# Optimization experiments

Measured on AMD Instinct MI355X. Metric: run time of the kernel, lower is better.

## Reference

```python
import jax, jax.numpy as jnp
import numpy as np

NEG_SLOPE = 0.2  # PyG GATConv default negative_slope


def gat_conv(x, src, dst, W, a_src, a_dst, b, n_nodes):
    # x: [N, Cin]; W: [H, Cin, Cout]; a_src/a_dst: [H, Cout]; b: [Cout]
    xh = jnp.einsum('ni,hio->nho', x, W)                 # [N, H, Cout]
    al_s = jnp.einsum('nho,ho->nh', xh, a_src)           # [N, H]
    al_d = jnp.einsum('nho,ho->nh', xh, a_dst)           # [N, H]
    e = jax.nn.leaky_relu(al_s[src] + al_d[dst], NEG_SLOPE)  # [E, H]
    # softmax over incoming edges of each dst node (self-loops guarantee >=1 edge)
    m = jax.ops.segment_max(e, dst, num_segments=n_nodes)
    ex = jnp.exp(e - m[dst])
    den = jax.ops.segment_sum(ex, dst, num_segments=n_nodes)
    alpha = ex / den[dst]                                # [E, H]
    msg = alpha[:, :, None] * xh[src]                    # [E, H, Cout]
    out = jax.ops.segment_sum(msg, dst, num_segments=n_nodes)  # [N, H, Cout]
    return out.mean(axis=1) + b                          # concat=False -> head mean


def setup_inputs() -> dict:
    key = jax.random.key(0)
    ks = jax.random.split(key, 16)
    N, E, C, H = 20000, 320000, 128, 4
    s = 1.0 / np.sqrt(C)
    inp = {
        'x': jax.random.normal(ks[0], (N, C), dtype=jnp.float32),
        'edge_index': jax.random.randint(ks[1], (2, E), 0, N, dtype=jnp.int64),
    }
    for i, name in enumerate(['1', '2', 'r']):
        k0, k1, k2 = jax.random.split(ks[2 + i], 3)
        inp['W' + name] = jax.random.normal(k0, (H, C, C), dtype=jnp.float32) * s
        inp['as' + name] = jax.random.normal(k1, (H, C), dtype=jnp.float32) * s
        inp['ad' + name] = jax.random.normal(k2, (H, C), dtype=jnp.float32) * s
        inp['b' + name] = jnp.zeros((C,), dtype=jnp.float32)
    return inp


def reference(x, edge_index, W1, as1, ad1, b1, W2, as2, ad2, b2, Wr, asr, adr, br):
    n = x.shape[0]
    loop = jnp.arange(n, dtype=edge_index.dtype)
    src = jnp.concatenate([edge_index[0], loop])  # PyG add_self_loops=True
    dst = jnp.concatenate([edge_index[1], loop])
    h = gat_conv(x, src, dst, W1, as1, ad1, b1, n)
    h = gat_conv(h, src, dst, W2, as2, ad2, b2, n)
    res = gat_conv(x, src, dst, Wr, asr, adr, br, n)
    return h + res
```

## Files before the change

kernel.cpp:

```cpp
#include <hip/hip_runtime.h>
#include <math.h>

#define C 128

typedef unsigned short u16;
typedef __attribute__((ext_vector_type(8))) short short8;
typedef __attribute__((ext_vector_type(4))) float f32x4;
typedef __attribute__((ext_vector_type(4))) u16 u16x4;

__device__ __forceinline__ float b2f(u16 u) {
    union { unsigned i; float f; } x; x.i = (unsigned)u << 16; return x.f;
}
__device__ __forceinline__ u16 f2b(float f) {
    union { float f; unsigned i; } x; x.f = f;
    unsigned r = x.i + 0x7FFFu + ((x.i >> 16) & 1u);
    return (u16)(r >> 16);
}
__device__ __forceinline__ float lrelu(float x) { return x > 0.f ? x : 0.2f * x; }


__global__ void hist_kernel(const int* __restrict__ ei, int E, int N,
                            int* __restrict__ count) {
    int total = E + N;
    for (int e = blockIdx.x * blockDim.x + threadIdx.x; e < total;
         e += gridDim.x * blockDim.x) {
        int d = (e < E) ? ei[E + e] : (e - E);
        if ((unsigned)d < (unsigned)N) atomicAdd(&count[d], 1);
    }
}

__global__ __launch_bounds__(1024) void scan_kernel(const int* __restrict__ count,
                                                    int* __restrict__ offs,
                                                    int* __restrict__ cursor, int N) {
    int tid = threadIdx.x, lane = tid & 63, wid = tid >> 6;
    int CH = (N + 1023) >> 10;
    int base = tid * CH;
    int s = 0;
    for (int j = 0; j < CH; ++j) {
        int i = base + j;
        if (i < N) s += count[i];
    }
    int own = s;
    #pragma unroll
    for (int d = 1; d < 64; d <<= 1) {
        int v = __shfl_up(s, d);
        if (lane >= d) s += v;
    }
    __shared__ int wtot[16];
    if (lane == 63) wtot[wid] = s;
    __syncthreads();
    if (tid < 16) {
        int t = wtot[tid];
        int u = t;
        #pragma unroll
        for (int d = 1; d < 16; d <<= 1) {
            int v = __shfl_up(u, d);
            if (tid >= d) u += v;
        }
        wtot[tid] = u - t;
        if (tid == 15) offs[N] = u;
    }
    __syncthreads();
    int run = wtot[wid] + s - own;
    for (int j = 0; j < CH; ++j) {
        int i = base + j;
        if (i < N) {
            offs[i] = run;
            cursor[i] = run;
            run += count[i];
        }
    }
}

__global__ void scatter_kernel(const int* __restrict__ ei, int E, int N,
                               int* __restrict__ cursor, int* __restrict__ srcs) {
    int total = E + N;
    for (int e = blockIdx.x * blockDim.x + threadIdx.x; e < total;
         e += gridDim.x * blockDim.x) {
        int sNode, d;
        if (e < E) { sNode = ei[e]; d = ei[E + e]; }
        else       { sNode = e - E; d = sNode; }
        if ((unsigned)d < (unsigned)N && (unsigned)sNode < (unsigned)N) {
            int pos = atomicAdd(&cursor[d], 1);
            srcs[pos] = sNode;
        }
    }
}


__global__ __launch_bounds__(256) void cvt_w_kernel(const float* __restrict__ W1,
                                                    const float* __restrict__ Wr,
                                                    const float* __restrict__ W2,
                                                    u16* __restrict__ Wf) {
    int idx = blockIdx.x * 256 + threadIdx.x;
    int lane = idx & 63;
    int kk = (idx >> 6) & 15;
    int t = (idx >> 10) & 7;
    int l = idx >> 13;
    if (l >= 3) return;
    const float* W = (l == 0) ? W1 : (l == 1) ? Wr : W2;
    int o = t * 16 + (lane & 15);
    int bk = kk * 32 + (lane >> 4) * 8;
    int h = bk >> 7, i0 = bk & 127;
    short8 v;
    #pragma unroll
    for (int j = 0; j < 8; ++j) {
        v[j] = (short)f2b(0.25f * W[((size_t)h * C + i0 + j) * C + o]);
    }
    *(short8*)(Wf + (size_t)idx * 8) = v;
}


__global__ __launch_bounds__(256) void wvec_kernel(const float* __restrict__ W1,
                                                   const float* __restrict__ as1,
                                                   const float* __restrict__ ad1,
                                                   const float* __restrict__ Wr,
                                                   const float* __restrict__ asr,
                                                   const float* __restrict__ adr,
                                                   const float* __restrict__ W2,
                                                   const float* __restrict__ as2,
                                                   const float* __restrict__ ad2,
                                                   u16* __restrict__ vsdA,
                                                   u16* __restrict__ vsdB) {
    int slot = blockIdx.x;
    const float* W  = (slot < 4) ? W1 : (slot < 8) ? Wr : W2;
    const float* s_ = (slot < 4) ? as1 : (slot < 8) ? asr : as2;
    const float* d_ = (slot < 4) ? ad1 : (slot < 8) ? adr : ad2;
    int h = slot & 3;
    int wave = threadIdx.x >> 6, lane = threadIdx.x & 63;
    int rbase = blockIdx.y * 32 + wave * 8;
    float as0 = s_[h * C + lane], as1v = s_[h * C + 64 + lane];
    float ad0 = d_[h * C + lane], ad1v = d_[h * C + 64 + lane];
    #pragma unroll
    for (int j = 0; j < 8; ++j) {
        int i = rbase + j;
        const float* Wrow = W + ((size_t)h * C + i) * C;
        float w0 = Wrow[lane], w1 = Wrow[64 + lane];
        float ps = w0 * as0 + w1 * as1v;
        float pd = w0 * ad0 + w1 * ad1v;
        #pragma unroll
        for (int m = 32; m; m >>= 1) {
            ps += __shfl_xor(ps, m);
            pd += __shfl_xor(pd, m);
        }
        if (lane == 0) {
            if (slot < 8) {
                vsdA[slot * C + i] = f2b(ps);
                vsdA[(8 + slot) * C + i] = f2b(pd);
            } else {
                vsdB[(slot - 8) * C + i] = f2b(ps);
                vsdB[(4 + (slot - 8)) * C + i] = f2b(pd);
            }
        }
    }
}


__global__ __launch_bounds__(256) void alA_kernel(const float* __restrict__ x,
                                                  const u16* __restrict__ vsd,
                                                  u16* __restrict__ xb,
                                                  float* __restrict__ als,
                                                  float* __restrict__ ald, int N) {
    int wave = threadIdx.x >> 6, lane = threadIdx.x & 63;
    int rowBase = blockIdx.x * 64 + wave * 16;
    int r = rowBase + (lane & 15);
    int rl = r < N ? r : N - 1;
    int kg = (lane >> 4) * 8;

    short8 a[4];
    #pragma unroll
    for (int t = 0; t < 4; ++t) {
        const float* xp = x + (size_t)rl * C + t * 32 + kg;
        float4 f0 = *(const float4*)xp;
        float4 f1 = *(const float4*)(xp + 4);
        short8 s;
        s[0] = f2b(f0.x); s[1] = f2b(f0.y); s[2] = f2b(f0.z); s[3] = f2b(f0.w);
        s[4] = f2b(f1.x); s[5] = f2b(f1.y); s[6] = f2b(f1.z); s[7] = f2b(f1.w);
        a[t] = s;
        if (r < N) *(short8*)(xb + (size_t)r * C + t * 32 + kg) = s;
    }
    f32x4 acc = {0.f, 0.f, 0.f, 0.f};
    int col = lane & 15;
    #pragma unroll
    for (int t = 0; t < 4; ++t) {
        short8 b = *(const short8*)(vsd + (size_t)col * C + t * 32 + kg);
        acc = __builtin_amdgcn_mfma_f32_16x16x32_bf16(a[t], b, acc, 0, 0, 0);
    }
    #pragma unroll
    for (int j = 0; j < 4; ++j) {
        int rr = rowBase + (lane >> 4) * 4 + j;
        if (rr < N) {
            if (col < 8) als[rr * 8 + col] = acc[j];
            else ald[rr * 8 + (col - 8)] = acc[j];
        }
    }
}


__global__ __launch_bounds__(256) void alB_kernel(const u16* __restrict__ in,
                                                  const u16* __restrict__ vsd,
                                                  float* __restrict__ als,
                                                  float* __restrict__ ald, int N) {
    int wave = threadIdx.x >> 6, lane = threadIdx.x & 63;
    int rowBase = blockIdx.x * 64 + wave * 16;
    int r = rowBase + (lane & 15);
    int rl = r < N ? r : N - 1;
    int kg = (lane >> 4) * 8;

    f32x4 acc = {0.f, 0.f, 0.f, 0.f};
    int col = lane & 15;
    #pragma unroll
    for (int t = 0; t < 4; ++t) {
        short8 a = *(const short8*)(in + (size_t)rl * C + t * 32 + kg);
        short8 b = *(const short8*)(vsd + (size_t)col * C + t * 32 + kg);
        acc = __builtin_amdgcn_mfma_f32_16x16x32_bf16(a, b, acc, 0, 0, 0);
    }
    #pragma unroll
    for (int j = 0; j < 4; ++j) {
        int rr = rowBase + (lane >> 4) * 4 + j;
        if (rr < N && col < 8) {
            if (col < 4) als[rr * 4 + col] = acc[j];
            else ald[rr * 4 + (col - 4)] = acc[j];
        }
    }
}


template <int NH>
__global__ __launch_bounds__(256) void denf_kernel(const float* __restrict__ als,
                                                   const float* __restrict__ ald,
                                                   const int* __restrict__ offs,
                                                   const int* __restrict__ srcs,
                                                   float* __restrict__ wgt,
                                                   float* __restrict__ den, int N) {
    int idx = blockIdx.x * blockDim.x + threadIdx.x;
    int node = idx / NH, h = idx % NH;
    if (node >= N) return;
    float adh = ald[(size_t)node * NH + h];
    int beg = offs[node], end = offs[node + 1];
    float s = 0.f;
    for (int i = beg; i < end; ++i) {
        float w = __expf(lrelu(als[(size_t)srcs[i] * NH + h] + adh));
        wgt[(size_t)i * NH + h] = w;
        s += w;
    }
    den[idx] = s;
}


template <int NH>
__global__ __launch_bounds__(256) void aggx_kernel(const u16* __restrict__ xsrc,
                                                   const float* __restrict__ wgt,
                                                   const float* __restrict__ den,
                                                   const int* __restrict__ offs,
                                                   const int* __restrict__ srcs,
                                                   u16* __restrict__ dest, int N) {
    constexpr int NHG = NH / 2;
    int node = blockIdx.x * 4 + (threadIdx.x >> 6);
    int lane = threadIdx.x & 63;
    if (node >= N) return;
    int g = lane >> 5;
    int c0 = (lane & 31) * 4;
    int beg = offs[node], end = offs[node + 1];

    float inv[NHG];
    #pragma unroll
    for (int j = 0; j < NHG; ++j) {
        inv[j] = 1.f / den[(size_t)node * NH + g * NHG + j];
    }

    float acc[NHG][4] = {};
    int i = beg;
    for (; i + 8 <= end; i += 8) {
        int s[8];
        #pragma unroll
        for (int e = 0; e < 8; ++e) s[e] = srcs[i + e];
        u16x4 v[8];
        #pragma unroll
        for (int e = 0; e < 8; ++e) {
            v[e] = *(const u16x4*)(xsrc + (size_t)s[e] * C + c0);
        }
        float wv[8][NHG];
        #pragma unroll
        for (int e = 0; e < 8; ++e) {
            if constexpr (NHG == 4) {
                float4 wq = *(const float4*)(wgt + (size_t)(i + e) * NH + g * NHG);
                wv[e][0] = wq.x; wv[e][1] = wq.y; wv[e][2] = wq.z; wv[e][3] = wq.w;
            } else {
                float2 wq = *(const float2*)(wgt + (size_t)(i + e) * NH + g * NHG);
                wv[e][0] = wq.x; wv[e][1] = wq.y;
            }
        }
        #pragma unroll
        for (int e = 0; e < 8; ++e) {
            float f[4];
            #pragma unroll
            for (int j = 0; j < 4; ++j) f[j] = b2f(v[e][j]);
            #pragma unroll
            for (int j2 = 0; j2 < NHG; ++j2) {
                #pragma unroll
                for (int j = 0; j < 4; ++j) acc[j2][j] += wv[e][j2] * f[j];
            }
        }
    }
    for (; i < end; ++i) {
        int s0 = srcs[i];
        u16x4 v0 = *(const u16x4*)(xsrc + (size_t)s0 * C + c0);
        float w0[NHG];
        #pragma unroll
        for (int j2 = 0; j2 < NHG; ++j2) {
            w0[j2] = wgt[(size_t)i * NH + g * NHG + j2];
        }
        float f[4];
        #pragma unroll
        for (int j = 0; j < 4; ++j) f[j] = b2f(v0[j]);
        #pragma unroll
        for (int j2 = 0; j2 < NHG; ++j2) {
            #pragma unroll
            for (int j = 0; j < 4; ++j) acc[j2][j] += w0[j2] * f[j];
        }
    }

    #pragma unroll
    for (int j2 = 0; j2 < NHG; ++j2) {
        int h = g * NHG + j2;
        u16x4 o = {f2b(acc[j2][0] * inv[j2]), f2b(acc[j2][1] * inv[j2]),
                   f2b(acc[j2][2] * inv[j2]), f2b(acc[j2][3] * inv[j2])};
        *(u16x4*)(dest + (size_t)node * (NH * C) + h * C + c0) = o;
    }
}


__global__ __launch_bounds__(256) void gemmL1_kernel(const u16* __restrict__ agg,
                                                     const u16* __restrict__ Wf,
                                                     const float* __restrict__ b1,
                                                     u16* __restrict__ h1b, int N) {
    int wave = threadIdx.x >> 6, lane = threadIdx.x & 63;
    int ch = blockIdx.y;
    int rowBase = blockIdx.x * 64 + wave * 16;
    int p = lane & 15, q = lane >> 4;
    int r = rowBase + p;
    int rl = r < N ? r : N - 1;
    int kg = q * 8;

    const short8* ap = (const short8*)(agg + (size_t)rl * 1024 + kg);
    const u16* wb = Wf + (size_t)(ch * 4 * 16) * 512 + lane * 8;

    f32x4 acc[4];
    #pragma unroll
    for (int t = 0; t < 4; ++t) acc[t] = (f32x4){0.f, 0.f, 0.f, 0.f};

    #pragma unroll
    for (int kk = 0; kk < 16; ++kk) {
        short8 a = ap[kk * 4];
        #pragma unroll
        for (int t = 0; t < 4; ++t) {
            short8 b = *(const short8*)(wb + (size_t)(t * 16 + kk) * 512);
            acc[t] = __builtin_amdgcn_mfma_f32_16x16x32_bf16(a, b, acc[t], 0, 0, 0);
        }
    }

    #pragma unroll
    for (int t = 0; t < 4; ++t) {
        int col = (ch * 4 + t) * 16 + p;
        float bcol = b1[col];
        #pragma unroll
        for (int j = 0; j < 4; ++j) {
            int rr = rowBase + q * 4 + j;
            if (rr < N) h1b[(size_t)rr * C + col] = f2b(acc[t][j] + bcol);
        }
    }
}


__global__ __launch_bounds__(256) void gemmF_kernel(const u16* __restrict__ aggB,
                                                    const u16* __restrict__ aggA,
                                                    const u16* __restrict__ Wf,
                                                    const float* __restrict__ b2,
                                                    const float* __restrict__ br,
                                                    float* __restrict__ outf, int N) {
    int wave = threadIdx.x >> 6, lane = threadIdx.x & 63;
    int ch = blockIdx.y;
    int rowBase = blockIdx.x * 64 + wave * 16;
    int p = lane & 15, q = lane >> 4;
    int r = rowBase + p;
    int rl = r < N ? r : N - 1;
    int kg = q * 8;

    const short8* apB = (const short8*)(aggB + (size_t)rl * 512 + kg);
    const short8* apR = (const short8*)(aggA + (size_t)rl * 1024 + 512 + kg);
    const u16* wb2 = Wf + (size_t)2 * 65536 + (size_t)(ch * 4 * 16) * 512 + lane * 8;
    const u16* wbr = Wf + (size_t)1 * 65536 + (size_t)(ch * 4 * 16) * 512 + lane * 8;

    f32x4 acc[4];
    #pragma unroll
    for (int t = 0; t < 4; ++t) acc[t] = (f32x4){0.f, 0.f, 0.f, 0.f};

    #pragma unroll
    for (int kk = 0; kk < 16; ++kk) {
        short8 a = apB[kk * 4];
        #pragma unroll
        for (int t = 0; t < 4; ++t) {
            short8 b = *(const short8*)(wb2 + (size_t)(t * 16 + kk) * 512);
            acc[t] = __builtin_amdgcn_mfma_f32_16x16x32_bf16(a, b, acc[t], 0, 0, 0);
        }
    }
    #pragma unroll
    for (int kk = 0; kk < 16; ++kk) {
        short8 a = apR[kk * 4];
        #pragma unroll
        for (int t = 0; t < 4; ++t) {
            short8 b = *(const short8*)(wbr + (size_t)(t * 16 + kk) * 512);
            acc[t] = __builtin_amdgcn_mfma_f32_16x16x32_bf16(a, b, acc[t], 0, 0, 0);
        }
    }

    #pragma unroll
    for (int t = 0; t < 4; ++t) {
        int col = (ch * 4 + t) * 16 + p;
        float bcol = b2[col] + br[col];
        #pragma unroll
        for (int j = 0; j < 4; ++j) {
            int rr = rowBase + q * 4 + j;
            if (rr < N) outf[(size_t)rr * C + col] = acc[t][j] + bcol;
        }
    }
}


extern "C" void kernel_launch(void* const* d_in, const int* in_sizes, int n_in,
                              void* d_out, int out_size, void* d_ws, size_t ws_size,
                              hipStream_t stream) {
    const float* x = (const float*)d_in[0];
    const int* ei = (const int*)d_in[1];
    const float* W1 = (const float*)d_in[2];
    const float* as1 = (const float*)d_in[3];
    const float* ad1 = (const float*)d_in[4];
    const float* b1 = (const float*)d_in[5];
    const float* W2 = (const float*)d_in[6];
    const float* as2 = (const float*)d_in[7];
    const float* ad2 = (const float*)d_in[8];
    const float* b2 = (const float*)d_in[9];
    const float* Wr = (const float*)d_in[10];
    const float* asr = (const float*)d_in[11];
    const float* adr = (const float*)d_in[12];
    const float* br = (const float*)d_in[13];

    int N = in_sizes[0] / C;
    int E = in_sizes[1] / 2;
    int ET = E + N;

    size_t sz_xb    = (size_t)N * C * 2;
    size_t sz_h1b   = (size_t)N * C * 2;
    size_t sz_aggA  = (size_t)N * 1024 * 2;
    size_t sz_aggB  = (size_t)N * 512 * 2;
    size_t sz_wc    = (size_t)3 * C * 512 * 2;
    size_t sz_vsd   = (size_t)16 * C * 2;
    size_t sz_al8   = (size_t)N * 8 * 4;
    size_t sz_count = (size_t)N * 4;
    size_t sz_den8  = (size_t)N * 8 * 4;
    size_t sz_den4  = (size_t)N * 4 * 4;
    size_t sz_offs  = (size_t)(N + 4) * 4;
    size_t sz_srcs  = (size_t)ET * 4;
    size_t sz_w     = (size_t)ET * 8 * 4;
    size_t required = sz_xb + sz_h1b + sz_aggA + sz_aggB + sz_wc + 2 * sz_vsd +
                      2 * sz_al8 + sz_count + sz_den8 + sz_den4 + sz_count +
                      sz_offs + 2 * sz_srcs + sz_w;
    if (ws_size < required) return;

    char* w = (char*)d_ws;
    u16* xb = (u16*)w;        w += sz_xb;
    u16* h1b = (u16*)w;       w += sz_h1b;
    u16* aggA = (u16*)w;      w += sz_aggA;
    u16* aggB = (u16*)w;      w += sz_aggB;
    u16* Wf = (u16*)w;        w += sz_wc;
    u16* vsdA = (u16*)w;      w += sz_vsd;
    u16* vsdB = (u16*)w;      w += sz_vsd;
    float* als = (float*)w;   w += sz_al8;
    float* ald = (float*)w;   w += sz_al8;
    int* count = (int*)w;     w += sz_count;
    float* den8 = (float*)w;  w += sz_den8;
    float* den4 = (float*)w;  w += sz_den4;
    int* cursor = (int*)w;    w += sz_count;
    int* offs = (int*)w;      w += sz_offs;
    int* srcs = (int*)w;      w += sz_srcs;
    w += sz_srcs;
    float* wgt = (float*)w;   w += sz_w;
    float* out = (float*)d_out;

    hipMemsetAsync(count, 0, sz_count, stream);
    hist_kernel<<<512, 256, 0, stream>>>(ei, E, N, count);
    scan_kernel<<<1, 1024, 0, stream>>>(count, offs, cursor, N);
    scatter_kernel<<<512, 256, 0, stream>>>(ei, E, N, cursor, srcs);

    cvt_w_kernel<<<96, 256, 0, stream>>>(W1, Wr, W2, Wf);
    wvec_kernel<<<dim3(12, 4), 256, 0, stream>>>(W1, as1, ad1, Wr, asr, adr,
                                                 W2, as2, ad2, vsdA, vsdB);

    int nwb = (N + 3) / 4;
    int gx = (N + 63) / 64;
    int nd8 = (N * 8 + 255) / 256;
    int nd4 = (N * 4 + 255) / 256;

    alA_kernel<<<gx, 256, 0, stream>>>(x, vsdA, xb, als, ald, N);
    denf_kernel<8><<<nd8, 256, 0, stream>>>(als, ald, offs, srcs, wgt, den8, N);
    aggx_kernel<8><<<nwb, 256, 0, stream>>>(xb, wgt, den8, offs, srcs, aggA, N);
    gemmL1_kernel<<<dim3(gx, 2), 256, 0, stream>>>(aggA, Wf, b1, h1b, N);

    alB_kernel<<<gx, 256, 0, stream>>>(h1b, vsdB, als, ald, N);
    denf_kernel<4><<<nd4, 256, 0, stream>>>(als, ald, offs, srcs, wgt, den4, N);
    aggx_kernel<4><<<nwb, 256, 0, stream>>>(h1b, wgt, den4, offs, srcs, aggB, N);
    gemmF_kernel<<<dim3(gx, 2), 256, 0, stream>>>(aggB, aggA, Wf, b2, br, out, N);
}
```

Measured before the change: 309.0 us.

## Compute edge weights per edge and fold softmax denominator into aggregation

Replaces the per-node denominator kernel, which serially walks each node's incoming edges, with a per-edge kernel that writes exp(leaky_relu) weights in parallel using a new dst array filled during scatter. The softmax denominator is now accumulated inside the aggregation kernel, which removes the den buffers and a dependent read. The aggregation loop also prefetches the next batch of source indices. The cost is an extra dst array write and read, plus redundant denominator sums across the lanes of each wave.

```diff
diff --git a/kernel.cpp b/kernel.cpp
--- a/kernel.cpp
+++ b/kernel.cpp
@@ -73,7 +73,8 @@
 }
 
 __global__ void scatter_kernel(const int* __restrict__ ei, int E, int N,
-                               int* __restrict__ cursor, int* __restrict__ srcs) {
+                               int* __restrict__ cursor, int* __restrict__ srcs,
+                               int* __restrict__ dsts) {
     int total = E + N;
     for (int e = blockIdx.x * blockDim.x + threadIdx.x; e < total;
          e += gridDim.x * blockDim.x) {
@@ -83,6 +84,7 @@
         if ((unsigned)d < (unsigned)N && (unsigned)sNode < (unsigned)N) {
             int pos = atomicAdd(&cursor[d], 1);
             srcs[pos] = sNode;
+            dsts[pos] = d;
         }
     }
 }
@@ -227,31 +229,27 @@
 
 
 template <int NH>
-__global__ __launch_bounds__(256) void denf_kernel(const float* __restrict__ als,
-                                                   const float* __restrict__ ald,
-                                                   const int* __restrict__ offs,
-                                                   const int* __restrict__ srcs,
-                                                   float* __restrict__ wgt,
-                                                   float* __restrict__ den, int N) {
-    int idx = blockIdx.x * blockDim.x + threadIdx.x;
-    int node = idx / NH, h = idx % NH;
-    if (node >= N) return;
-    float adh = ald[(size_t)node * NH + h];
-    int beg = offs[node], end = offs[node + 1];
-    float s = 0.f;
-    for (int i = beg; i < end; ++i) {
-        float w = __expf(lrelu(als[(size_t)srcs[i] * NH + h] + adh));
-        wgt[(size_t)i * NH + h] = w;
-        s += w;
-    }
-    den[idx] = s;
+__global__ __launch_bounds__(256) void ew_kernel(const float* __restrict__ als,
+                                                 const float* __restrict__ ald,
+                                                 const int* __restrict__ srcs,
+                                                 const int* __restrict__ dsts,
+                                                 float* __restrict__ wout, int ET) {
+    int i = blockIdx.x * blockDim.x + threadIdx.x;
+    if (i >= ET) return;
+    int s = srcs[i], d = dsts[i];
+    const float* as_ = als + (size_t)s * NH;
+    const float* ad_ = ald + (size_t)d * NH;
+    float* wo = wout + (size_t)i * NH;
+    #pragma unroll
+    for (int h = 0; h < NH; ++h) {
+        wo[h] = __expf(lrelu(as_[h] + ad_[h]));
+    }
 }
 
 
 template <int NH>
 __global__ __launch_bounds__(256) void aggx_kernel(const u16* __restrict__ xsrc,
                                                    const float* __restrict__ wgt,
-                                                   const float* __restrict__ den,
                                                    const int* __restrict__ offs,
                                                    const int* __restrict__ srcs,
                                                    u16* __restrict__ dest, int N) {
@@ -263,44 +261,53 @@
     int c0 = (lane & 31) * 4;
     int beg = offs[node], end = offs[node + 1];
 
-    float inv[NHG];
-    #pragma unroll
-    for (int j = 0; j < NHG; ++j) {
-        inv[j] = 1.f / den[(size_t)node * NH + g * NHG + j];
-    }
-
+    float dacc[NHG] = {};
     float acc[NHG][4] = {};
+
     int i = beg;
-    for (; i + 8 <= end; i += 8) {
-        int s[8];
-        #pragma unroll
-        for (int e = 0; e < 8; ++e) s[e] = srcs[i + e];
-        u16x4 v[8];
-        #pragma unroll
-        for (int e = 0; e < 8; ++e) {
-            v[e] = *(const u16x4*)(xsrc + (size_t)s[e] * C + c0);
-        }
-        float wv[8][NHG];
-        #pragma unroll
-        for (int e = 0; e < 8; ++e) {
-            if constexpr (NHG == 4) {
-                float4 wq = *(const float4*)(wgt + (size_t)(i + e) * NH + g * NHG);
-                wv[e][0] = wq.x; wv[e][1] = wq.y; wv[e][2] = wq.z; wv[e][3] = wq.w;
-            } else {
-                float2 wq = *(const float2*)(wgt + (size_t)(i + e) * NH + g * NHG);
-                wv[e][0] = wq.x; wv[e][1] = wq.y;
+    int iend8 = beg + ((end - beg) & ~7);
+
+    if (i < iend8) {
+        int sA[8];
+        #pragma unroll
+        for (int e = 0; e < 8; ++e) sA[e] = srcs[i + e];
+        while (i < iend8) {
+            int inext = i + 8;
+            int sB[8];
+            #pragma unroll
+            for (int e = 0; e < 8; ++e) sB[e] = srcs[inext + e];
+
+            u16x4 v[8];
+            #pragma unroll
+            for (int e = 0; e < 8; ++e) {
+                v[e] = *(const u16x4*)(xsrc + (size_t)sA[e] * C + c0);
             }
-        }
-        #pragma unroll
-        for (int e = 0; e < 8; ++e) {
-            float f[4];
+            float wv[8][NHG];
             #pragma unroll
-            for (int j = 0; j < 4; ++j) f[j] = b2f(v[e][j]);
+            for (int e = 0; e < 8; ++e) {
+                if constexpr (NHG == 4) {
+                    float4 wq = *(const float4*)(wgt + (size_t)(i + e) * NH + g * NHG);
+                    wv[e][0] = wq.x; wv[e][1] = wq.y; wv[e][2] = wq.z; wv[e][3] = wq.w;
+                } else {
+                    float2 wq = *(const float2*)(wgt + (size_t)(i + e) * NH + g * NHG);
+                    wv[e][0] = wq.x; wv[e][1] = wq.y;
+                }
+            }
             #pragma unroll
-            for (int j2 = 0; j2 < NHG; ++j2) {
+            for (int e = 0; e < 8; ++e) {
+                float f[4];
                 #pragma unroll
-                for (int j = 0; j < 4; ++j) acc[j2][j] += wv[e][j2] * f[j];
+                for (int j = 0; j < 4; ++j) f[j] = b2f(v[e][j]);
+                #pragma unroll
+                for (int j2 = 0; j2 < NHG; ++j2) {
+                    dacc[j2] += wv[e][j2];
+                    #pragma unroll
+                    for (int j = 0; j < 4; ++j) acc[j2][j] += wv[e][j2] * f[j];
+                }
             }
+            #pragma unroll
+            for (int e = 0; e < 8; ++e) sA[e] = sB[e];
+            i = inext;
         }
     }
     for (; i < end; ++i) {
@@ -316,6 +323,7 @@
         for (int j = 0; j < 4; ++j) f[j] = b2f(v0[j]);
         #pragma unroll
         for (int j2 = 0; j2 < NHG; ++j2) {
+            dacc[j2] += w0[j2];
             #pragma unroll
             for (int j = 0; j < 4; ++j) acc[j2][j] += w0[j2] * f[j];
         }
@@ -323,9 +331,10 @@
 
     #pragma unroll
     for (int j2 = 0; j2 < NHG; ++j2) {
+        float inv = 1.f / dacc[j2];
         int h = g * NHG + j2;
-        u16x4 o = {f2b(acc[j2][0] * inv[j2]), f2b(acc[j2][1] * inv[j2]),
-                   f2b(acc[j2][2] * inv[j2]), f2b(acc[j2][3] * inv[j2])};
+        u16x4 o = {f2b(acc[j2][0] * inv), f2b(acc[j2][1] * inv),
+                   f2b(acc[j2][2] * inv), f2b(acc[j2][3] * inv)};
         *(u16x4*)(dest + (size_t)node * (NH * C) + h * C + c0) = o;
     }
 }
@@ -458,14 +467,11 @@
     size_t sz_vsd   = (size_t)16 * C * 2;
     size_t sz_al8   = (size_t)N * 8 * 4;
     size_t sz_count = (size_t)N * 4;
-    size_t sz_den8  = (size_t)N * 8 * 4;
-    size_t sz_den4  = (size_t)N * 4 * 4;
     size_t sz_offs  = (size_t)(N + 4) * 4;
     size_t sz_srcs  = (size_t)ET * 4;
     size_t sz_w     = (size_t)ET * 8 * 4;
     size_t required = sz_xb + sz_h1b + sz_aggA + sz_aggB + sz_wc + 2 * sz_vsd +
-                      2 * sz_al8 + sz_count + sz_den8 + sz_den4 + sz_count +
-                      sz_offs + 2 * sz_srcs + sz_w;
+                      2 * sz_al8 + 2 * sz_count + sz_offs + 2 * sz_srcs + sz_w;
     if (ws_size < required) return;
 
     char* w = (char*)d_ws;
@@ -479,36 +485,33 @@
     float* als = (float*)w;   w += sz_al8;
     float* ald = (float*)w;   w += sz_al8;
     int* count = (int*)w;     w += sz_count;
-    float* den8 = (float*)w;  w += sz_den8;
-    float* den4 = (float*)w;  w += sz_den4;
     int* cursor = (int*)w;    w += sz_count;
     int* offs = (int*)w;      w += sz_offs;
     int* srcs = (int*)w;      w += sz_srcs;
-    w += sz_srcs;
+    int* dsts = (int*)w;      w += sz_srcs;
     float* wgt = (float*)w;   w += sz_w;
     float* out = (float*)d_out;
 
     hipMemsetAsync(count, 0, sz_count, stream);
     hist_kernel<<<512, 256, 0, stream>>>(ei, E, N, count);
     scan_kernel<<<1, 1024, 0, stream>>>(count, offs, cursor, N);
-    scatter_kernel<<<512, 256, 0, stream>>>(ei, E, N, cursor, srcs);
+    scatter_kernel<<<512, 256, 0, stream>>>(ei, E, N, cursor, srcs, dsts);
 
     cvt_w_kernel<<<96, 256, 0, stream>>>(W1, Wr, W2, Wf);
     wvec_kernel<<<dim3(12, 4), 256, 0, stream>>>(W1, as1, ad1, Wr, asr, adr,
                                                  W2, as2, ad2, vsdA, vsdB);
 
     int nwb = (N + 3) / 4;
+    int neb = (ET + 255) / 256;
     int gx = (N + 63) / 64;
-    int nd8 = (N * 8 + 255) / 256;
-    int nd4 = (N * 4 + 255) / 256;
 
     alA_kernel<<<gx, 256, 0, stream>>>(x, vsdA, xb, als, ald, N);
-    denf_kernel<8><<<nd8, 256, 0, stream>>>(als, ald, offs, srcs, wgt, den8, N);
-    aggx_kernel<8><<<nwb, 256, 0, stream>>>(xb, wgt, den8, offs, srcs, aggA, N);
+    ew_kernel<8><<<neb, 256, 0, stream>>>(als, ald, srcs, dsts, wgt, ET);
+    aggx_kernel<8><<<nwb, 256, 0, stream>>>(xb, wgt, offs, srcs, aggA, N);
     gemmL1_kernel<<<dim3(gx, 2), 256, 0, stream>>>(aggA, Wf, b1, h1b, N);
 
     alB_kernel<<<gx, 256, 0, stream>>>(h1b, vsdB, als, ald, N);
-    denf_kernel<4><<<nd4, 256, 0, stream>>>(als, ald, offs, srcs, wgt, den4, N);
-    aggx_kernel<4><<<nwb, 256, 0, stream>>>(h1b, wgt, den4, offs, srcs, aggB, N);
+    ew_kernel<4><<<neb, 256, 0, stream>>>(als, ald, srcs, dsts, wgt, ET);
+    aggx_kernel<4><<<nwb, 256, 0, stream>>>(h1b, wgt, offs, srcs, aggB, N);
     gemmF_kernel<<<dim3(gx, 2), 256, 0, stream>>>(aggB, aggA, Wf, b2, br, out, N);
 }
```

After: 307.8 us. Within noise of the previous version (-0.4%).
